# Optimization experiments

Measured on AMD Instinct MI355X. Metric: run time of the kernel, lower is better.

The kernel has to match this reference:

```python
import jax, jax.numpy as jnp
import numpy as np

INPUT, HIDDEN, OUTPUT = 256, 512, 64
B, T = 128, 256

def gru_layer(x, W_ih, W_hh, b_ih, b_hh):
    # x: [B, T, in]; W_ih: [3H, in]; W_hh: [3H, H]; gate order r, z, n (PyTorch)
    Bv = x.shape[0]
    H = W_hh.shape[1]
    xg = jnp.einsum('bti,gi->btg', x, W_ih) + b_ih  # precompute input gates [B,T,3H]

    def step(h, xg_t):
        hg = h @ W_hh.T + b_hh
        xr, xz, xn = jnp.split(xg_t, 3, axis=-1)
        hr, hz, hn = jnp.split(hg, 3, axis=-1)
        r = jax.nn.sigmoid(xr + hr)
        z = jax.nn.sigmoid(xz + hz)
        n = jnp.tanh(xn + r * hn)
        h_new = (1.0 - z) * n + z * h
        return h_new, h_new

    h0 = jnp.zeros((Bv, H), x.dtype)
    _, ys = jax.lax.scan(step, h0, jnp.swapaxes(xg, 0, 1))  # [T,B,H]
    return jnp.swapaxes(ys, 0, 1)  # [B,T,H]

def setup_inputs() -> dict:
    key = jax.random.key(0)
    ks = jax.random.split(key, 12)
    s_in = 1.0 / np.sqrt(HIDDEN)
    inp = {
        'x': jax.random.normal(ks[0], (B, T, INPUT), dtype=jnp.float32),
        'W_ih0': jax.random.uniform(ks[1], (3 * HIDDEN, INPUT), minval=-s_in, maxval=s_in),
        'W_hh0': jax.random.uniform(ks[2], (3 * HIDDEN, HIDDEN), minval=-s_in, maxval=s_in),
        'b_ih0': jax.random.uniform(ks[3], (3 * HIDDEN,), minval=-s_in, maxval=s_in),
        'b_hh0': jax.random.uniform(ks[4], (3 * HIDDEN,), minval=-s_in, maxval=s_in),
        'W_ih1': jax.random.uniform(ks[5], (3 * HIDDEN, HIDDEN), minval=-s_in, maxval=s_in),
        'W_hh1': jax.random.uniform(ks[6], (3 * HIDDEN, HIDDEN), minval=-s_in, maxval=s_in),
        'b_ih1': jax.random.uniform(ks[7], (3 * HIDDEN,), minval=-s_in, maxval=s_in),
        'b_hh1': jax.random.uniform(ks[8], (3 * HIDDEN,), minval=-s_in, maxval=s_in),
        'W_out': jax.random.uniform(ks[9], (OUTPUT, HIDDEN), minval=-s_in, maxval=s_in),
        'b_out': jax.random.uniform(ks[10], (OUTPUT,), minval=-s_in, maxval=s_in),
    }
    return inp

def reference(x, W_ih0, W_hh0, b_ih0, b_hh0, W_ih1, W_hh1, b_ih1, b_hh1, W_out, b_out):
    h = gru_layer(x, W_ih0, W_hh0, b_ih0, b_hh0)   # layer 0
    h = gru_layer(h, W_ih1, W_hh1, b_ih1, b_hh1)   # layer 1 (dropout=0.0 -> no-op)
    last = h[:, -1, :]                              # [B, H]
    yhat = last @ W_out.T + b_out                   # [B, OUTPUT]
    return yhat
```

## Files before the change

kernel.cpp:

```cpp
#include <hip/hip_runtime.h>
#include <hip/hip_bf16.h>
#include <stdint.h>

typedef __attribute__((ext_vector_type(8))) __bf16 bf16x8;
typedef __attribute__((ext_vector_type(4))) float  floatx4;

#define T_STEPS 256
#define BATCH   128
#define HID     512

__device__ __forceinline__ float sigmoidf_(float x) { return 1.f / (1.f + __expf(-x)); }
__device__ __forceinline__ float tanhf_(float y) {
  float e = __expf(-2.f * fabsf(y));
  return copysignf((1.f - e) / (1.f + e), y);
}

template <int SLP>
__device__ __forceinline__ void pollline_(const int* base, int target) {
  while (1) {
    int v = __hip_atomic_load(base, __ATOMIC_RELAXED, __HIP_MEMORY_SCOPE_AGENT);
    if (__all(v >= target)) break;
    __builtin_amdgcn_s_sleep(SLP);
  }
  asm volatile("" ::: "memory");
}

__global__ __launch_bounds__(256) void gru_fused(
    const float* __restrict__ x,
    const float* __restrict__ Wih0, const float* __restrict__ Whh0,
    const float* __restrict__ bih0, const float* __restrict__ bhh0,
    const float* __restrict__ Wih1, const float* __restrict__ Whh1,
    const float* __restrict__ bih1, const float* __restrict__ bhh1,
    __bf16* __restrict__ h0base,
    __bf16* __restrict__ h1base,
    int* __restrict__ fl)
{
  const int tid   = threadIdx.x;
  const int layer = blockIdx.x >> 7;
  const int bg    = (blockIdx.x >> 6) & 1;
  const int g     = blockIdx.x & 63;
  const int w = tid >> 6, l = tid & 63, c = l & 15, q = l >> 4;
  const int Kin = layer ? HID : 256;
  const int KTx = Kin >> 5;
  const int KT  = KTx + 16;
  const int rowbase = bg * 64 + w * 16;
  const int jj  = g * 8 + c;

  const float* Wih = layer ? Wih1 : Wih0;
  const float* Whh = layer ? Whh1 : Whh0;
  const float* bih = layer ? bih1 : bih0;
  const float* bhh = layer ? bhh1 : bhh0;
  __bf16* hbase = layer ? h1base : h0base;

  __shared__ __bf16 ldsW[2 * 32 * 64 * 8];

  for (int cid = tid; cid < 2 * KT * 64; cid += 256) {
    int nt = cid / (KT * 64);
    int r1 = cid - nt * (KT * 64);
    int kt = r1 >> 6;
    int ll = r1 & 63;
    int cc = ll & 15, qq = ll >> 4;
    int k  = kt * 32 + qq * 8;
    int grow;
    if (nt == 0) grow = (cc < 8) ? (g * 8 + cc) : (512 + g * 8 + (cc - 8));
    else         grow = (cc < 8) ? (1024 + g * 8 + cc) : -1;
    bf16x8 v;
    if (grow >= 0) {
      const float* src = (k < Kin) ? (Wih + (size_t)grow * Kin + k)
                                   : (Whh + (size_t)grow * HID + (k - Kin));
      #pragma unroll
      for (int j = 0; j < 8; ++j) v[j] = (__bf16)src[j];
    } else {
      #pragma unroll
      for (int j = 0; j < 8; ++j) v[j] = (__bf16)0.f;
    }
    *(bf16x8*)&ldsW[((size_t)(nt * KT + kt) * 64 + ll) * 8] = v;
  }
  __syncthreads();

  bf16x8 WH[16][2];
  #pragma unroll
  for (int kt = 0; kt < 16; ++kt) {
    WH[kt][0] = *(const bf16x8*)&ldsW[((size_t)(0 * KT + KTx + kt) * 64 + l) * 8];
    WH[kt][1] = *(const bf16x8*)&ldsW[((size_t)(1 * KT + KTx + kt) * 64 + l) * 8];
  }

  float bias0, bias_nx, bias_nh;
  if (c < 8) {
    bias0   = bih[jj] + bhh[jj];
    bias_nx = bih[1024 + jj];
    bias_nh = bhh[1024 + jj];
  } else {
    int j2 = g * 8 + (c - 8);
    bias0   = bih[512 + j2] + bhh[512 + j2];
    bias_nx = 0.f; bias_nh = 0.f;
  }

  floatx4 accA[2], accB[2];
  const floatx4 zero4 = {0.f, 0.f, 0.f, 0.f};
  float hprev[4] = {0.f, 0.f, 0.f, 0.f};

  int* fpost      = fl + ((size_t)((layer * 2 + bg) * 64 + g)) * 32;
  const int* fown = fl + ((size_t)((layer * 2 + bg) * 64 + l)) * 32;
  const int* fx   = fl + ((size_t)(bg * 64 + l)) * 32;

  auto hslab = [&](int t) -> __bf16* {
    return hbase + (size_t)t * (BATCH * HID);
  };

  auto phaseX = [&](int t) {
    accA[0] = zero4; accA[1] = zero4;
    if (layer == 0) {
      const float* xp = x + ((size_t)(rowbase + c) * T_STEPS + t) * 256 + q * 8;
      for (int kt = 0; kt < 8; ++kt) {
        bf16x8 b0 = *(const bf16x8*)&ldsW[((size_t)(0 * KT + kt) * 64 + l) * 8];
        bf16x8 b1 = *(const bf16x8*)&ldsW[((size_t)(1 * KT + kt) * 64 + l) * 8];
        floatx4 u = *(const floatx4*)(xp + kt * 32);
        floatx4 v = *(const floatx4*)(xp + kt * 32 + 4);
        bf16x8 a;
        a[0] = (__bf16)u[0]; a[1] = (__bf16)u[1]; a[2] = (__bf16)u[2]; a[3] = (__bf16)u[3];
        a[4] = (__bf16)v[0]; a[5] = (__bf16)v[1]; a[6] = (__bf16)v[2]; a[7] = (__bf16)v[3];
        accA[0] = __builtin_amdgcn_mfma_f32_16x16x32_bf16(a, b0, accA[0], 0, 0, 0);
        accA[1] = __builtin_amdgcn_mfma_f32_16x16x32_bf16(a, b1, accA[1], 0, 0, 0);
      }
    } else {
      const __bf16* xp = h0base + (size_t)t * (BATCH * HID)
                       + (size_t)(rowbase + c) * HID + q * 8;
      for (int kt = 0; kt < 16; ++kt) {
        bf16x8 b0 = *(const bf16x8*)&ldsW[((size_t)(0 * KT + kt) * 64 + l) * 8];
        bf16x8 b1 = *(const bf16x8*)&ldsW[((size_t)(1 * KT + kt) * 64 + l) * 8];
        bf16x8 a = *(const bf16x8*)(xp + kt * 32);
        accA[0] = __builtin_amdgcn_mfma_f32_16x16x32_bf16(a, b0, accA[0], 0, 0, 0);
        accA[1] = __builtin_amdgcn_mfma_f32_16x16x32_bf16(a, b1, accA[1], 0, 0, 0);
      }
    }
  };

  if (layer == 1) pollline_<2>(fx, 1);
  phaseX(0);

  for (int t = 0; t < T_STEPS; ++t) {
    accB[0] = zero4; accB[1] = zero4;
    if (t > 0) {
      const __bf16* hA = hslab(t - 1) + (size_t)(rowbase + c) * HID + q * 8;
      bf16x8 hfrag[16];
      #pragma unroll
      for (int kt = 0; kt < 16; ++kt)
        hfrag[kt] = *(const bf16x8*)(hA + kt * 32);
      #pragma unroll
      for (int kt = 0; kt < 16; ++kt) {
        accB[0] = __builtin_amdgcn_mfma_f32_16x16x32_bf16(hfrag[kt], WH[kt][0], accB[0], 0, 0, 0);
        accB[1] = __builtin_amdgcn_mfma_f32_16x16x32_bf16(hfrag[kt], WH[kt][1], accB[1], 0, 0, 0);
      }
    }

    __bf16* hs = hslab(t);
    #pragma unroll
    for (int rg = 0; rg < 4; ++rg) {
      float pre0 = accA[0][rg] + accB[0][rg] + bias0;
      float zs = __shfl(pre0, (l & 48) | ((c + 8) & 15), 64);
      float r  = sigmoidf_(pre0);
      float z  = sigmoidf_(zs);
      float nn = tanhf_(accA[1][rg] + bias_nx + r * (accB[1][rg] + bias_nh));
      float hnew = (1.f - z) * nn + z * hprev[rg];
      hprev[rg] = hnew;
      unsigned short us = __builtin_bit_cast(unsigned short, (__bf16)hnew);
      int po = __shfl_xor((int)us, 1, 64);
      if (c < 8 && (c & 1) == 0) {
        uint32_t v = (uint32_t)us | ((uint32_t)po << 16);
        int row = rowbase + q * 4 + rg;
        __hip_atomic_store((uint32_t*)(hs + (size_t)row * HID + jj), v,
                           __ATOMIC_RELAXED, __HIP_MEMORY_SCOPE_AGENT);
      }
    }

    asm volatile("s_waitcnt vmcnt(0)" ::: "memory");
    __syncthreads();
    if (tid == 0)
      __hip_atomic_store(fpost, t + 1, __ATOMIC_RELAXED, __HIP_MEMORY_SCOPE_AGENT);

    if (t + 1 < T_STEPS) {
      if (layer == 1) pollline_<2>(fx, t + 2);
      phaseX(t + 1);
      pollline_<1>(fown, t + 1);
    }
  }
}

__global__ __launch_bounds__(64) void outproj(const __bf16* __restrict__ h1,
                                              const float* __restrict__ Wout,
                                              const float* __restrict__ bout,
                                              float* __restrict__ out) {
  int b = blockIdx.x, o = threadIdx.x;
  const __bf16* hr = h1 + (size_t)b * HID;
  const float*  wr = Wout + (size_t)o * HID;
  float acc = bout[o];
  for (int k = 0; k < HID; k += 8) {
    bf16x8 h8 = *(const bf16x8*)(hr + k);
    #pragma unroll
    for (int j = 0; j < 8; ++j) acc += (float)h8[j] * wr[k + j];
  }
  out[b * 64 + o] = acc;
}

extern "C" void kernel_launch(void* const* d_in, const int* in_sizes, int n_in,
                              void* d_out, int out_size, void* d_ws, size_t ws_size,
                              hipStream_t stream) {
  const float* x    = (const float*)d_in[0];
  const float* Wih0 = (const float*)d_in[1];
  const float* Whh0 = (const float*)d_in[2];
  const float* bih0 = (const float*)d_in[3];
  const float* bhh0 = (const float*)d_in[4];
  const float* Wih1 = (const float*)d_in[5];
  const float* Whh1 = (const float*)d_in[6];
  const float* bih1 = (const float*)d_in[7];
  const float* bhh1 = (const float*)d_in[8];
  const float* Wout = (const float*)d_in[9];
  const float* bout = (const float*)d_in[10];

  char* ws = (char*)d_ws;
  __bf16* h0 = (__bf16*)(ws);
  __bf16* h1 = (__bf16*)(ws + (32u << 20));
  int*    fl = (int*)(ws + (64u << 20));

  (void)hipMemsetAsync(fl, 0, 2 * 2 * 64 * 32 * 4, stream);

  gru_fused<<<256, 256, 0, stream>>>(x,
                                     Wih0, Whh0, bih0, bhh0,
                                     Wih1, Whh1, bih1, bhh1,
                                     h0, h1, fl);

  outproj<<<128, 64, 0, stream>>>(h1 + (size_t)255 * BATCH * HID,
                                  Wout, bout, (float*)d_out);
}
```

Measured before the change: 1.707 ms.

## Replace layer-0→layer-1 flag polling with sentinel-filled data polling

Layer 1 no longer polls layer-0 completion flags before consuming h0. Instead, the h0 buffer is pre-filled with a sentinel pattern and layer 1 reloads each 16-byte fragment with cache-bypassing loads until no word equals the sentinel. This removes a flag round-trip from the cross-layer dependency so data and readiness arrive together. In exchange it adds a 32 MB memset per launch. It also relies on the computed bf16 pairs never matching the sentinel and on 16-byte stores being seen whole, since each fragment is built from 4-byte stores made by different producer blocks.

```diff
diff --git a/kernel.cpp b/kernel.cpp
--- a/kernel.cpp
+++ b/kernel.cpp
@@ -4,15 +4,45 @@
 
 typedef __attribute__((ext_vector_type(8))) __bf16 bf16x8;
 typedef __attribute__((ext_vector_type(4))) float  floatx4;
+typedef __attribute__((ext_vector_type(4))) unsigned int uintx4;
 
 #define T_STEPS 256
 #define BATCH   128
 #define HID     512
+#define SENTW 0x7F7F7F7Fu
 
 __device__ __forceinline__ float sigmoidf_(float x) { return 1.f / (1.f + __expf(-x)); }
 __device__ __forceinline__ float tanhf_(float y) {
   float e = __expf(-2.f * fabsf(y));
   return copysignf((1.f - e) / (1.f + e), y);
+}
+
+__device__ __forceinline__ bool okw_(uintx4 w) {
+  return (w[0] != SENTW) & (w[1] != SENTW) & (w[2] != SENTW) & (w[3] != SENTW);
+}
+
+__device__ __forceinline__ void sentload16_(const __bf16* base, uintx4* hw) {
+  unsigned pend = 0xFFFFu;
+  while (pend) {
+    #pragma unroll
+    for (int kt = 0; kt < 16; ++kt)
+      if (pend & (1u << kt)) {
+        const void* p = (const void*)(base + kt * 32);
+        asm volatile("global_load_dwordx4 %0, %1, off sc0 sc1"
+                     : "=v"(hw[kt]) : "v"(p));
+      }
+    asm volatile("s_waitcnt vmcnt(0)" ::: "memory");
+    __builtin_amdgcn_sched_barrier(0);
+    unsigned np = 0;
+    #pragma unroll
+    for (int kt = 0; kt < 16; ++kt)
+      if (pend & (1u << kt)) {
+        if (!okw_(hw[kt])) np |= (1u << kt);
+      }
+    pend = np;
+    if (pend == 0xFFFFu) __builtin_amdgcn_s_sleep(4);
+    else if (pend)       __builtin_amdgcn_s_sleep(1);
+  }
 }
 
 template <int SLP>
@@ -102,7 +132,6 @@
 
   int* fpost      = fl + ((size_t)((layer * 2 + bg) * 64 + g)) * 32;
   const int* fown = fl + ((size_t)((layer * 2 + bg) * 64 + l)) * 32;
-  const int* fx   = fl + ((size_t)(bg * 64 + l)) * 32;
 
   auto hslab = [&](int t) -> __bf16* {
     return hbase + (size_t)t * (BATCH * HID);
@@ -126,17 +155,19 @@
     } else {
       const __bf16* xp = h0base + (size_t)t * (BATCH * HID)
                        + (size_t)(rowbase + c) * HID + q * 8;
+      uintx4 aw[16];
+      sentload16_(xp, aw);
+      #pragma unroll
       for (int kt = 0; kt < 16; ++kt) {
         bf16x8 b0 = *(const bf16x8*)&ldsW[((size_t)(0 * KT + kt) * 64 + l) * 8];
         bf16x8 b1 = *(const bf16x8*)&ldsW[((size_t)(1 * KT + kt) * 64 + l) * 8];
-        bf16x8 a = *(const bf16x8*)(xp + kt * 32);
+        bf16x8 a  = __builtin_bit_cast(bf16x8, aw[kt]);
         accA[0] = __builtin_amdgcn_mfma_f32_16x16x32_bf16(a, b0, accA[0], 0, 0, 0);
         accA[1] = __builtin_amdgcn_mfma_f32_16x16x32_bf16(a, b1, accA[1], 0, 0, 0);
       }
     }
   };
 
-  if (layer == 1) pollline_<2>(fx, 1);
   phaseX(0);
 
   for (int t = 0; t < T_STEPS; ++t) {
@@ -180,7 +211,6 @@
       __hip_atomic_store(fpost, t + 1, __ATOMIC_RELAXED, __HIP_MEMORY_SCOPE_AGENT);
 
     if (t + 1 < T_STEPS) {
-      if (layer == 1) pollline_<2>(fx, t + 2);
       phaseX(t + 1);
       pollline_<1>(fown, t + 1);
     }
@@ -223,6 +253,7 @@
   __bf16* h1 = (__bf16*)(ws + (32u << 20));
   int*    fl = (int*)(ws + (64u << 20));
 
+  (void)hipMemsetAsync(h0, 0x7F, (32u << 20), stream);
   (void)hipMemsetAsync(fl, 0, 2 * 2 * 64 * 32 * 4, stream);
 
   gru_fused<<<256, 256, 0, stream>>>(x,
```

After: 2.048 ms. 1.2x slower.

## Prefetch next-step input activations into registers before gate computation

Applied to the files above, without the earlier changes.

Issues the loads of the next timestep's input (x for layer 0, layer-0 hidden slab for layer 1) into a register buffer before the gate math and hidden-state stores, so their latency overlaps the current step's work. The layer-1 flag poll is made speculative: an asynchronous flag load is issued after the input projection and only checked before the prefetch, falling back to polling if not ready. This adds 16 vector registers of prefetch state and inline asm loads, raising register pressure and adding ordering subtleties around the flag.

```diff
diff --git a/kernel.cpp b/kernel.cpp
--- a/kernel.cpp
+++ b/kernel.cpp
@@ -99,6 +99,8 @@
   floatx4 accA[2], accB[2];
   const floatx4 zero4 = {0.f, 0.f, 0.f, 0.f};
   float hprev[4] = {0.f, 0.f, 0.f, 0.f};
+  floatx4 pf[16];
+  int vfx = 0x7fffffff;
 
   int* fpost      = fl + ((size_t)((layer * 2 + bg) * 64 + g)) * 32;
   const int* fown = fl + ((size_t)((layer * 2 + bg) * 64 + l)) * 32;
@@ -108,10 +110,10 @@
     return hbase + (size_t)t * (BATCH * HID);
   };
 
-  auto phaseX = [&](int t) {
+  auto phaseX0 = [&]() {
     accA[0] = zero4; accA[1] = zero4;
     if (layer == 0) {
-      const float* xp = x + ((size_t)(rowbase + c) * T_STEPS + t) * 256 + q * 8;
+      const float* xp = x + ((size_t)(rowbase + c) * T_STEPS + 0) * 256 + q * 8;
       for (int kt = 0; kt < 8; ++kt) {
         bf16x8 b0 = *(const bf16x8*)&ldsW[((size_t)(0 * KT + kt) * 64 + l) * 8];
         bf16x8 b1 = *(const bf16x8*)&ldsW[((size_t)(1 * KT + kt) * 64 + l) * 8];
@@ -124,8 +126,7 @@
         accA[1] = __builtin_amdgcn_mfma_f32_16x16x32_bf16(a, b1, accA[1], 0, 0, 0);
       }
     } else {
-      const __bf16* xp = h0base + (size_t)t * (BATCH * HID)
-                       + (size_t)(rowbase + c) * HID + q * 8;
+      const __bf16* xp = h0base + (size_t)(rowbase + c) * HID + q * 8;
       for (int kt = 0; kt < 16; ++kt) {
         bf16x8 b0 = *(const bf16x8*)&ldsW[((size_t)(0 * KT + kt) * 64 + l) * 8];
         bf16x8 b1 = *(const bf16x8*)&ldsW[((size_t)(1 * KT + kt) * 64 + l) * 8];
@@ -137,7 +138,9 @@
   };
 
   if (layer == 1) pollline_<2>(fx, 1);
-  phaseX(0);
+  phaseX0();
+  if (layer == 1)
+    asm volatile("global_load_dword %0, %1, off sc0 sc1" : "=v"(vfx) : "v"(fx));
 
   for (int t = 0; t < T_STEPS; ++t) {
     accB[0] = zero4; accB[1] = zero4;
@@ -151,6 +154,26 @@
       for (int kt = 0; kt < 16; ++kt) {
         accB[0] = __builtin_amdgcn_mfma_f32_16x16x32_bf16(hfrag[kt], WH[kt][0], accB[0], 0, 0, 0);
         accB[1] = __builtin_amdgcn_mfma_f32_16x16x32_bf16(hfrag[kt], WH[kt][1], accB[1], 0, 0, 0);
+      }
+    }
+
+    if (t + 1 < T_STEPS) {
+      if (layer == 0) {
+        const float* xp = x + ((size_t)(rowbase + c) * T_STEPS + (t + 1)) * 256 + q * 8;
+        #pragma unroll
+        for (int kt = 0; kt < 8; ++kt) {
+          pf[2 * kt]     = *(const floatx4*)(xp + kt * 32);
+          pf[2 * kt + 1] = *(const floatx4*)(xp + kt * 32 + 4);
+        }
+      } else {
+        asm volatile("s_waitcnt vmcnt(0)" : "+v"(vfx) :: "memory");
+        __builtin_amdgcn_sched_barrier(0);
+        if (!__all(vfx >= t + 2)) pollline_<2>(fx, t + 2);
+        const __bf16* xp = h0base + (size_t)(t + 1) * (BATCH * HID)
+                         + (size_t)(rowbase + c) * HID + q * 8;
+        #pragma unroll
+        for (int kt = 0; kt < 16; ++kt)
+          pf[kt] = *(const floatx4*)(xp + kt * 32);
       }
     }
 
@@ -180,8 +203,30 @@
       __hip_atomic_store(fpost, t + 1, __ATOMIC_RELAXED, __HIP_MEMORY_SCOPE_AGENT);
 
     if (t + 1 < T_STEPS) {
-      if (layer == 1) pollline_<2>(fx, t + 2);
-      phaseX(t + 1);
+      accA[0] = zero4; accA[1] = zero4;
+      if (layer == 0) {
+        #pragma unroll
+        for (int kt = 0; kt < 8; ++kt) {
+          bf16x8 b0 = *(const bf16x8*)&ldsW[((size_t)(0 * KT + kt) * 64 + l) * 8];
+          bf16x8 b1 = *(const bf16x8*)&ldsW[((size_t)(1 * KT + kt) * 64 + l) * 8];
+          floatx4 u = pf[2 * kt], v = pf[2 * kt + 1];
+          bf16x8 a;
+          a[0] = (__bf16)u[0]; a[1] = (__bf16)u[1]; a[2] = (__bf16)u[2]; a[3] = (__bf16)u[3];
+          a[4] = (__bf16)v[0]; a[5] = (__bf16)v[1]; a[6] = (__bf16)v[2]; a[7] = (__bf16)v[3];
+          accA[0] = __builtin_amdgcn_mfma_f32_16x16x32_bf16(a, b0, accA[0], 0, 0, 0);
+          accA[1] = __builtin_amdgcn_mfma_f32_16x16x32_bf16(a, b1, accA[1], 0, 0, 0);
+        }
+      } else {
+        #pragma unroll
+        for (int kt = 0; kt < 16; ++kt) {
+          bf16x8 b0 = *(const bf16x8*)&ldsW[((size_t)(0 * KT + kt) * 64 + l) * 8];
+          bf16x8 b1 = *(const bf16x8*)&ldsW[((size_t)(1 * KT + kt) * 64 + l) * 8];
+          bf16x8 a = __builtin_bit_cast(bf16x8, pf[kt]);
+          accA[0] = __builtin_amdgcn_mfma_f32_16x16x32_bf16(a, b0, accA[0], 0, 0, 0);
+          accA[1] = __builtin_amdgcn_mfma_f32_16x16x32_bf16(a, b1, accA[1], 0, 0, 0);
+        }
+        asm volatile("global_load_dword %0, %1, off sc0 sc1" : "=v"(vfx) : "v"(fx));
+      }
       pollline_<1>(fown, t + 1);
     }
   }
```

Result: slower. 1.761 ms (+3.1%).
